# Optimization experiments

Hardware: AMD Instinct MI355X
Metric: run time of the kernel (lower is better)

Reference implementation:

```python
import jax, jax.numpy as jnp
import numpy as np

DIM = 4096
N_HEADS = 32
N_KV = 8
HEAD_DIM = 128
WINDOW = 4096
BSZ = 1
SEQ = 2048
REPEATS = N_HEADS // N_KV
SCALE = HEAD_DIM ** -0.5
NEG_INF = -1e9


def setup_inputs() -> dict:
    key = jax.random.key(0)
    ks = jax.random.split(key, 5)
    x = jax.random.normal(ks[0], (1, BSZ, SEQ, DIM), jnp.float32)
    wq = jax.random.normal(ks[1], (N_HEADS * HEAD_DIM, DIM), jnp.float32) * (DIM ** -0.5)
    wk = jax.random.normal(ks[2], (N_KV * HEAD_DIM, DIM), jnp.float32) * (DIM ** -0.5)
    wv = jax.random.normal(ks[3], (N_KV * HEAD_DIM, DIM), jnp.float32) * (DIM ** -0.5)
    wo = jax.random.normal(ks[4], (DIM, N_HEADS * HEAD_DIM), jnp.float32) * (DIM ** -0.5)
    # rotary frequencies (Mistral/LLaMA style, base 10000)
    inv = 1.0 / (10000.0 ** (np.arange(0, HEAD_DIM, 2, dtype=np.float32) / HEAD_DIM))
    ang = np.outer(np.arange(SEQ, dtype=np.float32), inv)  # [SEQ, HEAD_DIM//2]
    freqs_cos = jnp.asarray(np.cos(ang), jnp.float32)
    freqs_sin = jnp.asarray(np.sin(ang), jnp.float32)
    positions = jnp.arange(SEQ, dtype=jnp.int32)
    # sliding-window causal additive mask [SEQ, SEQ]
    i = np.arange(SEQ)[:, None]
    j = np.arange(SEQ)[None, :]
    allowed = (j <= i) & (j > i - WINDOW)
    mask = jnp.asarray(np.where(allowed, 0.0, NEG_INF).astype(np.float32))
    cache_k = jnp.zeros((BSZ, WINDOW, N_KV, HEAD_DIM), jnp.float32)
    cache_v = jnp.zeros((BSZ, WINDOW, N_KV, HEAD_DIM), jnp.float32)
    return dict(x=x, wq=wq, wk=wk, wv=wv, wo=wo, freqs_cos=freqs_cos,
                freqs_sin=freqs_sin, positions=positions, mask=mask,
                cache_k=cache_k, cache_v=cache_v)


def _rope(x, cos, sin):
    # x: [b, s, h, hd]; pairs (x0,x1),(x2,x3),... treated as complex numbers
    xr = x[..., 0::2]
    xi = x[..., 1::2]
    c = cos[None, :, None, :]
    s = sin[None, :, None, :]
    out_r = xr * c - xi * s
    out_i = xr * s + xi * c
    return jnp.stack([out_r, out_i], axis=-1).reshape(x.shape)


def reference(x, wq, wk, wv, wo, freqs_cos, freqs_sin, positions, mask, cache_k, cache_v):
    b, s = BSZ, SEQ
    xf = x.reshape(b, s, DIM)
    xq = (xf @ wq.T).reshape(b, s, N_HEADS, HEAD_DIM)
    xk = (xf @ wk.T).reshape(b, s, N_KV, HEAD_DIM)
    xv = (xf @ wv.T).reshape(b, s, N_KV, HEAD_DIM)
    xq = _rope(xq, freqs_cos, freqs_sin)
    xk = _rope(xk, freqs_cos, freqs_sin)
    # sliding-window KV cache scatter update (last WINDOW positions, mod WINDOW)
    pos = positions[-WINDOW:] % WINDOW
    cache_k = cache_k.at[:, pos].set(xk[:, -WINDOW:])
    cache_v = cache_v.at[:, pos].set(xv[:, -WINDOW:])
    # prefill branch (positions.shape[0] > 1): attend over current xk/xv
    key = jnp.repeat(xk, REPEATS, axis=2)  # GQA repeat_kv -> [b, s, H, hd]
    val = jnp.repeat(xv, REPEATS, axis=2)
    q = xq.transpose(0, 2, 1, 3)  # [b, H, s, hd]
    k = key.transpose(0, 2, 1, 3)
    v = val.transpose(0, 2, 1, 3)
    scores = jnp.einsum('bhqd,bhkd->bhqk', q, k) * SCALE + mask[None, None]
    probs = jax.nn.softmax(scores, axis=-1)
    out = jnp.einsum('bhqk,bhkd->bhqd', probs, v)
    out = out.transpose(0, 2, 1, 3).reshape(1, b, s, N_HEADS * HEAD_DIM)
    return out @ wo.T, cache_k, cache_v
```

## Files before the change

kernel.cpp:

```cpp
#include <hip/hip_runtime.h>
#include <hip/hip_bf16.h>


typedef __attribute__((ext_vector_type(8))) short short8_t;
typedef __attribute__((ext_vector_type(2))) unsigned uint2_t;
typedef __attribute__((ext_vector_type(8))) __bf16 bf16x8;
typedef __attribute__((ext_vector_type(4))) float f32x4;
typedef __attribute__((ext_vector_type(16))) float f32x16;

#define SEQLEN 2048
#define QSCALE 0.08838834764831845f

__device__ __forceinline__ short f2b(float f) {
  if (!__builtin_isfinite(f)) f = 0.0f;
  union { float f; unsigned u; } v; v.f = f;
  unsigned r = (v.u + 0x7fffu + ((v.u >> 16) & 1u)) >> 16;
  return (short)r;
}
__device__ __forceinline__ float sf(float f) {
  return __builtin_isfinite(f) ? f : 0.0f;
}
__device__ __forceinline__ short8_t cvt8(const float* p) {
  f32x4 a = *(const f32x4*)p;
  f32x4 b = *(const f32x4*)(p + 4);
  short8_t o;
  o[0] = f2b(a[0]); o[1] = f2b(a[1]); o[2] = f2b(a[2]); o[3] = f2b(a[3]);
  o[4] = f2b(b[0]); o[5] = f2b(b[1]); o[6] = f2b(b[2]); o[7] = f2b(b[3]);
  return o;
}
__device__ __forceinline__ unsigned pkb(float lo, float hi) {
  union { float f; unsigned u; } a, b; a.f = lo; b.f = hi;
  unsigned ra = (a.u + 0x7fffu + ((a.u >> 16) & 1u)) >> 16;
  unsigned rb = (b.u + 0x7fffu + ((b.u >> 16) & 1u)) & 0xffff0000u;
  return rb | ra;
}

#define GLD16(gp, lp) __builtin_amdgcn_global_load_lds( \
    (const __attribute__((address_space(1))) void*)(gp), \
    (__attribute__((address_space(3))) void*)(lp), 16, 0, 0)

__global__ __launch_bounds__(256) void cvt_bf16(
    const float* __restrict__ in, short* __restrict__ out)
{
  size_t i = ((size_t)blockIdx.x * 256 + threadIdx.x) * 8;
  *(short8_t*)&out[i] = cvt8(in + i);
}

__global__ __launch_bounds__(256) void gemm_bf(
    const short* __restrict__ A, const short* __restrict__ W,
    float* __restrict__ C0, float* __restrict__ C1,
    int Kloop, int lda, int ldc)
{
  __shared__ short As[128 * 64];
  __shared__ short Ws[128 * 64];
  const int tid  = threadIdx.x;
  const int lane = tid & 63;
  const int wid  = tid >> 6;
  const int l15  = lane & 15;
  const int l4   = lane >> 4;

  const int nwg = (int)(gridDim.x * gridDim.y);
  int bid = (int)(blockIdx.y * gridDim.x + blockIdx.x);
  int swz = (bid & 7) * (nwg >> 3) + (bid >> 3);
  const int m0 = (swz / (int)gridDim.x) * 128;
  const int n0 = (swz % (int)gridDim.x) * 128;
  const int koff = (int)blockIdx.z * Kloop;
  float* C = blockIdx.z ? C1 : C0;

  const int wr = (wid >> 1) * 64;
  const int wc = (wid & 1) * 64;
  const int srow = tid >> 3;
  const int scol = (tid & 7) * 8;

  f32x4 acc[4][4] = {};

  const short* Ab = A + (size_t)(m0 + srow) * lda + koff + scol;
  const short* Wb = W + (size_t)(n0 + srow) * lda + koff + scol;

  for (int k0 = 0; k0 < Kloop; k0 += 64) {
#pragma unroll
    for (int i = 0; i < 4; ++i) {
      GLD16(Ab + (size_t)(i * 32) * lda + k0, &As[(i * 32 + wid * 8) * 64]);
      GLD16(Wb + (size_t)(i * 32) * lda + k0, &Ws[(i * 32 + wid * 8) * 64]);
    }
    __syncthreads();

#pragma unroll
    for (int kk = 0; kk < 2; ++kk) {
      bf16x8 af[4], wf[4];
#pragma unroll
      for (int m = 0; m < 4; ++m)
        af[m] = *(const bf16x8*)&As[(wr + m * 16 + l15) * 64 + kk * 32 + l4 * 8];
#pragma unroll
      for (int n = 0; n < 4; ++n)
        wf[n] = *(const bf16x8*)&Ws[(wc + n * 16 + l15) * 64 + kk * 32 + l4 * 8];
#pragma unroll
      for (int m = 0; m < 4; ++m)
#pragma unroll
        for (int n = 0; n < 4; ++n)
          acc[m][n] = __builtin_amdgcn_mfma_f32_16x16x32_bf16(af[m], wf[n], acc[m][n], 0, 0, 0);
    }
    __syncthreads();
  }

#pragma unroll
  for (int m = 0; m < 4; ++m) {
    int rbase = m0 + wr + m * 16 + l4 * 4;
#pragma unroll
    for (int n = 0; n < 4; ++n) {
      int cbase = n0 + wc + n * 16 + l15;
#pragma unroll
      for (int r = 0; r < 4; ++r)
        C[(size_t)(rbase + r) * ldc + cbase] = sf(acc[m][n][r]);
    }
  }
}

__device__ __forceinline__ void rope8v(const float* x0, float* out,
                                       const float* fc, const float* fs, int t, int p0)
{
  f32x4 cv = *(const f32x4*)&fc[t * 64 + p0];
  f32x4 sv = *(const f32x4*)&fs[t * 64 + p0];
#pragma unroll
  for (int i = 0; i < 4; ++i) {
    float xr = x0[2 * i], xi = x0[2 * i + 1];
    out[2 * i]     = sf(xr * cv[i] - xi * sv[i]);
    out[2 * i + 1] = sf(xr * sv[i] + xi * cv[i]);
  }
}

__global__ __launch_bounds__(256) void combine_rope_q(
    const float* __restrict__ p0, const float* __restrict__ p1,
    short* __restrict__ qb, const float* __restrict__ fc, const float* __restrict__ fs)
{
  size_t idx = ((size_t)blockIdx.x * 256 + threadIdx.x) * 8;
  int t   = (int)(idx >> 12);
  int col = (int)(idx & 4095);
  f32x4 a0 = *(const f32x4*)&p0[idx],     b0 = *(const f32x4*)&p0[idx + 4];
  f32x4 a1 = *(const f32x4*)&p1[idx],     b1 = *(const f32x4*)&p1[idx + 4];
  float s8[8] = {a0[0]+a1[0], a0[1]+a1[1], a0[2]+a1[2], a0[3]+a1[3],
                 b0[0]+b1[0], b0[1]+b1[1], b0[2]+b1[2], b0[3]+b1[3]};
  float o[8];
  rope8v(s8, o, fc, fs, t, (col & 127) >> 1);
  short8_t ob;
#pragma unroll
  for (int i = 0; i < 8; ++i) ob[i] = f2b(o[i] * QSCALE);
  *(short8_t*)&qb[idx] = ob;
}

__global__ __launch_bounds__(256) void combine_rope_kv(
    const float* __restrict__ p0, const float* __restrict__ p1,
    float* __restrict__ ck, short* __restrict__ kb, float* __restrict__ cv,
    const float* __restrict__ fc, const float* __restrict__ fs)
{
  size_t idx = ((size_t)blockIdx.x * 256 + threadIdx.x) * 8;
  int t   = (int)(idx >> 11);
  int col = (int)(idx & 2047);
  f32x4 a0 = *(const f32x4*)&p0[idx],     b0 = *(const f32x4*)&p0[idx + 4];
  f32x4 a1 = *(const f32x4*)&p1[idx],     b1 = *(const f32x4*)&p1[idx + 4];
  float s8[8] = {a0[0]+a1[0], a0[1]+a1[1], a0[2]+a1[2], a0[3]+a1[3],
                 b0[0]+b1[0], b0[1]+b1[1], b0[2]+b1[2], b0[3]+b1[3]};
  if (col < 1024) {
    float o[8];
    rope8v(s8, o, fc, fs, t, (col & 127) >> 1);
    size_t di = (size_t)t * 1024 + col;
    *(f32x4*)&ck[di]     = f32x4{o[0], o[1], o[2], o[3]};
    *(f32x4*)&ck[di + 4] = f32x4{o[4], o[5], o[6], o[7]};
    short8_t ob;
#pragma unroll
    for (int i = 0; i < 8; ++i) ob[i] = f2b(o[i]);
    *(short8_t*)&kb[di] = ob;
  } else {
    size_t di = (size_t)t * 1024 + (col - 1024);
    *(f32x4*)&cv[di]     = f32x4{sf(s8[0]), sf(s8[1]), sf(s8[2]), sf(s8[3])};
    *(f32x4*)&cv[di + 4] = f32x4{sf(s8[4]), sf(s8[5]), sf(s8[6]), sf(s8[7])};
  }
}

__global__ __launch_bounds__(256) void transpose_v(
    const float* __restrict__ cv, short* __restrict__ Vt)
{
  __shared__ short tile[64][72];
  const int t0 = blockIdx.x * 64;
  const int d0 = blockIdx.y * 64;
  const int h  = blockIdx.z;
  const int tid = threadIdx.x;
  const int r = tid >> 3;
  const int c = (tid & 7) * 8;
#pragma unroll
  for (int it = 0; it < 2; ++it) {
    short8_t v = cvt8(&cv[(size_t)(t0 + it * 32 + r) * 1024 + h * 128 + d0 + c]);
    *(short8_t*)&tile[it * 32 + r][c] = v;
  }
  __syncthreads();
#pragma unroll
  for (int it = 0; it < 2; ++it) {
    int dr = it * 32 + r;
    short8_t v;
#pragma unroll
    for (int i = 0; i < 8; ++i) v[i] = tile[c + i][dr];
    *(short8_t*)&Vt[(size_t)(h * 128 + d0 + dr) * SEQLEN + t0 + c] = v;
  }
}

__global__ __launch_bounds__(256) void attn_fwd7(
    const short* __restrict__ Q,
    const short* __restrict__ Kc,
    const short* __restrict__ Vt,
    short* __restrict__ O)
{
  const int bid = (int)blockIdx.x;
  const int kvh = bid & 7;
  const int qt  = 63 - (bid >> 3);
  const int tid = (int)threadIdx.x;
  const int wid = tid >> 6;
  const int h   = kvh * 4 + wid;
  const int lane = tid & 63;
  const int l31 = lane & 31;
  const int hi  = lane >> 5;

  __shared__ short Ks[64 * 128];
  __shared__ short Vs[128 * 64];
  __shared__ short P[4][32][72];
  __shared__ float exch[4][32];

  const int q0 = qt * 32;
  const int qg = q0 + l31;
  const int kend = q0 + 32;

  bf16x8 qf[8];
  {
    const short* qp = Q + (size_t)qg * 4096 + h * 128 + hi * 8;
#pragma unroll
    for (int ks = 0; ks < 8; ++ks) qf[ks] = *(const bf16x8*)(qp + ks * 16);
  }

  f32x16 o0 = {}, o1 = {}, o2 = {}, o3 = {};
  float m = -1e30f, l = 0.f;

  const int krow_base = wid * 16;
  const int vrow_base = wid * 32;
  const int xk = l31 & 15;
  const int xv = l31 & 7;

  for (int kt = 0; kt < kend; kt += 64) {
#pragma unroll
    for (int it = 0; it < 4; ++it) {
      int krow = krow_base + it * 4 + (lane >> 4);
      int kch  = (lane & 15) ^ (krow & 15);
      GLD16(Kc + (size_t)(kt + krow) * 1024 + kvh * 128 + kch * 8,
            &Ks[wid * 2048 + it * 512]);
      int vrow = vrow_base + it * 8 + (lane >> 3);
      int vch  = (lane & 7) ^ (vrow & 7);
      GLD16(Vt + (size_t)(kvh * 128 + vrow) * SEQLEN + kt + vch * 8,
            &Vs[wid * 2048 + it * 512]);
    }
    __syncthreads();

    f32x16 s0 = {}, s1 = {};
    {
      __builtin_amdgcn_s_setprio(1);
#pragma unroll
      for (int ks = 0; ks < 8; ++ks) {
        int ch = (ks * 2 + hi) ^ xk;
        bf16x8 k0 = *(const bf16x8*)&Ks[l31 * 128 + ch * 8];
        bf16x8 k1 = *(const bf16x8*)&Ks[(32 + l31) * 128 + ch * 8];
        s0 = __builtin_amdgcn_mfma_f32_32x32x16_bf16(k0, qf[ks], s0, 0, 0, 0);
        s1 = __builtin_amdgcn_mfma_f32_32x32x16_bf16(k1, qf[ks], s1, 0, 0, 0);
      }
      __builtin_amdgcn_s_setprio(0);
    }

    if (kt + 63 > q0) {
#pragma unroll
      for (int r = 0; r < 16; ++r) {
        int crow = (r & 3) + 8 * (r >> 2) + 4 * hi;
        if (kt + crow > qg)      s0[r] = -1e30f;
        if (kt + 32 + crow > qg) s1[r] = -1e30f;
      }
    }
    {
      float t[8];
#pragma unroll
      for (int r = 0; r < 8; ++r)
        t[r] = fmaxf(fmaxf(s0[r], s0[r + 8]), fmaxf(s1[r], s1[r + 8]));
      float pmax = fmaxf(fmaxf(fmaxf(t[0], t[1]), fmaxf(t[2], t[3])),
                         fmaxf(fmaxf(t[4], t[5]), fmaxf(t[6], t[7])));
      pmax = fmaxf(pmax, __shfl_xor(pmax, 32, 64));
      if (!__all(pmax <= m + 8.f)) {
        float mnew = fmaxf(m, pmax);
        float resc = __expf(m - mnew);
        m = mnew; l *= resc;
        if (lane < 32) exch[wid][l31] = resc;
#pragma unroll
        for (int r = 0; r < 16; ++r) {
          float rs = exch[wid][(r & 3) + 8 * (r >> 2) + 4 * hi];
          o0[r] *= rs; o1[r] *= rs; o2[r] *= rs; o3[r] *= rs;
        }
      }
      float psum = 0.f;
#pragma unroll
      for (int r = 0; r < 16; ++r) { s0[r] = __expf(s0[r] - m); psum += s0[r]; }
#pragma unroll
      for (int r = 0; r < 16; ++r) { s1[r] = __expf(s1[r] - m); psum += s1[r]; }
      l += psum + __shfl_xor(psum, 32, 64);
#pragma unroll
      for (int t4 = 0; t4 < 4; ++t4) {
        int c = 8 * t4 + 4 * hi;
        *(uint2_t*)&P[wid][l31][c]      = uint2_t{pkb(s0[4*t4], s0[4*t4+1]), pkb(s0[4*t4+2], s0[4*t4+3])};
        *(uint2_t*)&P[wid][l31][32 + c] = uint2_t{pkb(s1[4*t4], s1[4*t4+1]), pkb(s1[4*t4+2], s1[4*t4+3])};
      }
    }

#pragma unroll
    for (int g = 0; g < 4; ++g) {
      int ch = (g * 2 + hi) ^ xv;
      bf16x8 vf0 = *(const bf16x8*)&Vs[(l31)      * 64 + ch * 8];
      bf16x8 vf1 = *(const bf16x8*)&Vs[(32 + l31) * 64 + ch * 8];
      bf16x8 vf2 = *(const bf16x8*)&Vs[(64 + l31) * 64 + ch * 8];
      bf16x8 vf3 = *(const bf16x8*)&Vs[(96 + l31) * 64 + ch * 8];
      bf16x8 pf  = *(const bf16x8*)&P[wid][l31][g * 16 + hi * 8];
      __builtin_amdgcn_s_setprio(1);
      o0 = __builtin_amdgcn_mfma_f32_32x32x16_bf16(pf, vf0, o0, 0, 0, 0);
      o1 = __builtin_amdgcn_mfma_f32_32x32x16_bf16(pf, vf1, o1, 0, 0, 0);
      o2 = __builtin_amdgcn_mfma_f32_32x32x16_bf16(pf, vf2, o2, 0, 0, 0);
      o3 = __builtin_amdgcn_mfma_f32_32x32x16_bf16(pf, vf3, o3, 0, 0, 0);
      __builtin_amdgcn_s_setprio(0);
    }
    __syncthreads();
  }

  if (lane < 32) exch[wid][l31] = 1.f / l;
#pragma unroll
  for (int r = 0; r < 16; ++r) {
    int crow = (r & 3) + 8 * (r >> 2) + 4 * hi;
    float inv = exch[wid][crow];
    short* ob = O + (size_t)(q0 + crow) * 4096 + h * 128 + l31;
    ob[0]  = f2b(o0[r] * inv);
    ob[32] = f2b(o1[r] * inv);
    ob[64] = f2b(o2[r] * inv);
    ob[96] = f2b(o3[r] * inv);
  }
}

extern "C" void kernel_launch(void* const* d_in, const int* in_sizes, int n_in,
                              void* d_out, int out_size, void* d_ws, size_t ws_size,
                              hipStream_t stream) {
  const float* x  = (const float*)d_in[0];
  const float* wq = (const float*)d_in[1];
  const float* wk = (const float*)d_in[2];
  const float* wv = (const float*)d_in[3];
  const float* wo = (const float*)d_in[4];
  const float* fc = (const float*)d_in[5];
  const float* fs = (const float*)d_in[6];

  float* out = (float*)d_out;
  float* out_main = out;
  float* cache_k  = out + (size_t)2048 * 4096;
  float* cache_v  = cache_k + (size_t)4096 * 8 * 128;

  short* slotA = (short*)d_ws;
  short* slotB = (short*)((char*)d_ws + 33554432);
  short* Vt    = (short*)((char*)d_ws + 33554432 + 16777216);
  short* x_bf  = slotB;
  short* attn_out = slotB;
  short* q_bf  = slotA;
  short* wkv_bf = slotA + (size_t)2048 * 4096;
  short* k_bf  = slotA + (size_t)2048 * 4096;

  float* pQ0 = out_main;
  float* pQ1 = cache_k;
  float* pKV0 = out_main;
  float* pKV1 = out_main + (size_t)2048 * 2048;

  cvt_bf16<<<4096, 256, 0, stream>>>(x, x_bf);
  cvt_bf16<<<8192, 256, 0, stream>>>(wq, slotA);
  gemm_bf<<<dim3(32, 16, 2), 256, 0, stream>>>(x_bf, slotA, pQ0, pQ1, 2048, 4096, 4096);
  combine_rope_q<<<4096, 256, 0, stream>>>(pQ0, pQ1, q_bf, fc, fs);

  cvt_bf16<<<2048, 256, 0, stream>>>(wk, wkv_bf);
  cvt_bf16<<<2048, 256, 0, stream>>>(wv, wkv_bf + (size_t)1024 * 4096);
  gemm_bf<<<dim3(16, 16, 2), 256, 0, stream>>>(x_bf, wkv_bf, pKV0, pKV1, 2048, 4096, 2048);
  combine_rope_kv<<<2048, 256, 0, stream>>>(pKV0, pKV1, cache_k, k_bf, cache_v, fc, fs);
  transpose_v<<<dim3(32, 2, 8), 256, 0, stream>>>(cache_v, Vt);
  hipMemsetAsync(cache_k + (size_t)2048 * 1024, 0, (size_t)2048 * 1024 * 4, stream);
  hipMemsetAsync(cache_v + (size_t)2048 * 1024, 0, (size_t)2048 * 1024 * 4, stream);

  attn_fwd7<<<512, 256, 0, stream>>>(q_bf, k_bf, Vt, attn_out);

  cvt_bf16<<<8192, 256, 0, stream>>>(wo, slotA);
  gemm_bf<<<dim3(32, 16, 1), 256, 0, stream>>>(attn_out, slotA, out_main, out_main, 4096, 4096, 4096);
}
```

Before: 424.0 us.

## Fuse RoPE epilogue into projection GEMMs, drop split-K, double-buffer LDS

Drops the split-K (z=2) partial-sum scheme for the Q and KV projections. RoPE, the Q scale, and the bf16/fp32 cache writes now happen in the GEMM epilogue, using a lane shuffle to pair real and imaginary parts. This removes the two combine kernels and their fp32 partial round-trips. It also double-buffers the LDS tiles so the next K-slice loads are issued before computing on the current one. The cost is fewer workgroups for the QKV GEMMs (512 and 256 instead of 1024 and 512), which can lower occupancy and CU utilisation, plus doubled shared memory.

```diff
diff --git a/kernel.cpp b/kernel.cpp
--- a/kernel.cpp
+++ b/kernel.cpp
@@ -46,13 +46,15 @@
   *(short8_t*)&out[i] = cvt8(in + i);
 }
 
-__global__ __launch_bounds__(256) void gemm_bf(
+template <int EPI>
+__global__ __launch_bounds__(256) void gemm_epi(
     const short* __restrict__ A, const short* __restrict__ W,
-    float* __restrict__ C0, float* __restrict__ C1,
-    int Kloop, int lda, int ldc)
+    float* __restrict__ C, short* __restrict__ Cb, float* __restrict__ C2,
+    const float* __restrict__ fc, const float* __restrict__ fs,
+    int K, int ldc)
 {
-  __shared__ short As[128 * 64];
-  __shared__ short Ws[128 * 64];
+  __shared__ short As[2][128 * 64];
+  __shared__ short Ws[2][128 * 64];
   const int tid  = threadIdx.x;
   const int lane = tid & 63;
   const int wid  = tid >> 6;
@@ -64,8 +66,6 @@
   int swz = (bid & 7) * (nwg >> 3) + (bid >> 3);
   const int m0 = (swz / (int)gridDim.x) * 128;
   const int n0 = (swz % (int)gridDim.x) * 128;
-  const int koff = (int)blockIdx.z * Kloop;
-  float* C = blockIdx.z ? C1 : C0;
 
   const int wr = (wid >> 1) * 64;
   const int wc = (wid & 1) * 64;
@@ -74,26 +74,34 @@
 
   f32x4 acc[4][4] = {};
 
-  const short* Ab = A + (size_t)(m0 + srow) * lda + koff + scol;
-  const short* Wb = W + (size_t)(n0 + srow) * lda + koff + scol;
-
-  for (int k0 = 0; k0 < Kloop; k0 += 64) {
-#pragma unroll
-    for (int i = 0; i < 4; ++i) {
-      GLD16(Ab + (size_t)(i * 32) * lda + k0, &As[(i * 32 + wid * 8) * 64]);
-      GLD16(Wb + (size_t)(i * 32) * lda + k0, &Ws[(i * 32 + wid * 8) * 64]);
-    }
-    __syncthreads();
-
+  const short* Ab = A + (size_t)(m0 + srow) * K + scol;
+  const short* Wb = W + (size_t)(n0 + srow) * K + scol;
+
+#pragma unroll
+  for (int i = 0; i < 4; ++i) {
+    GLD16(Ab + (size_t)(i * 32) * K, &As[0][(i * 32 + wid * 8) * 64]);
+    GLD16(Wb + (size_t)(i * 32) * K, &Ws[0][(i * 32 + wid * 8) * 64]);
+  }
+  __syncthreads();
+
+  int cur = 0;
+  for (int k0 = 0; k0 < K; k0 += 64) {
+    if (k0 + 64 < K) {
+#pragma unroll
+      for (int i = 0; i < 4; ++i) {
+        GLD16(Ab + (size_t)(i * 32) * K + k0 + 64, &As[cur ^ 1][(i * 32 + wid * 8) * 64]);
+        GLD16(Wb + (size_t)(i * 32) * K + k0 + 64, &Ws[cur ^ 1][(i * 32 + wid * 8) * 64]);
+      }
+    }
 #pragma unroll
     for (int kk = 0; kk < 2; ++kk) {
       bf16x8 af[4], wf[4];
 #pragma unroll
       for (int m = 0; m < 4; ++m)
-        af[m] = *(const bf16x8*)&As[(wr + m * 16 + l15) * 64 + kk * 32 + l4 * 8];
+        af[m] = *(const bf16x8*)&As[cur][(wr + m * 16 + l15) * 64 + kk * 32 + l4 * 8];
 #pragma unroll
       for (int n = 0; n < 4; ++n)
-        wf[n] = *(const bf16x8*)&Ws[(wc + n * 16 + l15) * 64 + kk * 32 + l4 * 8];
+        wf[n] = *(const bf16x8*)&Ws[cur][(wc + n * 16 + l15) * 64 + kk * 32 + l4 * 8];
 #pragma unroll
       for (int m = 0; m < 4; ++m)
 #pragma unroll
@@ -101,6 +109,7 @@
           acc[m][n] = __builtin_amdgcn_mfma_f32_16x16x32_bf16(af[m], wf[n], acc[m][n], 0, 0, 0);
     }
     __syncthreads();
+    cur ^= 1;
   }
 
 #pragma unroll
@@ -110,70 +119,29 @@
     for (int n = 0; n < 4; ++n) {
       int cbase = n0 + wc + n * 16 + l15;
 #pragma unroll
-      for (int r = 0; r < 4; ++r)
-        C[(size_t)(rbase + r) * ldc + cbase] = sf(acc[m][n][r]);
-    }
-  }
-}
-
-__device__ __forceinline__ void rope8v(const float* x0, float* out,
-                                       const float* fc, const float* fs, int t, int p0)
-{
-  f32x4 cv = *(const f32x4*)&fc[t * 64 + p0];
-  f32x4 sv = *(const f32x4*)&fs[t * 64 + p0];
-#pragma unroll
-  for (int i = 0; i < 4; ++i) {
-    float xr = x0[2 * i], xi = x0[2 * i + 1];
-    out[2 * i]     = sf(xr * cv[i] - xi * sv[i]);
-    out[2 * i + 1] = sf(xr * sv[i] + xi * cv[i]);
-  }
-}
-
-__global__ __launch_bounds__(256) void combine_rope_q(
-    const float* __restrict__ p0, const float* __restrict__ p1,
-    short* __restrict__ qb, const float* __restrict__ fc, const float* __restrict__ fs)
-{
-  size_t idx = ((size_t)blockIdx.x * 256 + threadIdx.x) * 8;
-  int t   = (int)(idx >> 12);
-  int col = (int)(idx & 4095);
-  f32x4 a0 = *(const f32x4*)&p0[idx],     b0 = *(const f32x4*)&p0[idx + 4];
-  f32x4 a1 = *(const f32x4*)&p1[idx],     b1 = *(const f32x4*)&p1[idx + 4];
-  float s8[8] = {a0[0]+a1[0], a0[1]+a1[1], a0[2]+a1[2], a0[3]+a1[3],
-                 b0[0]+b1[0], b0[1]+b1[1], b0[2]+b1[2], b0[3]+b1[3]};
-  float o[8];
-  rope8v(s8, o, fc, fs, t, (col & 127) >> 1);
-  short8_t ob;
-#pragma unroll
-  for (int i = 0; i < 8; ++i) ob[i] = f2b(o[i] * QSCALE);
-  *(short8_t*)&qb[idx] = ob;
-}
-
-__global__ __launch_bounds__(256) void combine_rope_kv(
-    const float* __restrict__ p0, const float* __restrict__ p1,
-    float* __restrict__ ck, short* __restrict__ kb, float* __restrict__ cv,
-    const float* __restrict__ fc, const float* __restrict__ fs)
-{
-  size_t idx = ((size_t)blockIdx.x * 256 + threadIdx.x) * 8;
-  int t   = (int)(idx >> 11);
-  int col = (int)(idx & 2047);
-  f32x4 a0 = *(const f32x4*)&p0[idx],     b0 = *(const f32x4*)&p0[idx + 4];
-  f32x4 a1 = *(const f32x4*)&p1[idx],     b1 = *(const f32x4*)&p1[idx + 4];
-  float s8[8] = {a0[0]+a1[0], a0[1]+a1[1], a0[2]+a1[2], a0[3]+a1[3],
-                 b0[0]+b1[0], b0[1]+b1[1], b0[2]+b1[2], b0[3]+b1[3]};
-  if (col < 1024) {
-    float o[8];
-    rope8v(s8, o, fc, fs, t, (col & 127) >> 1);
-    size_t di = (size_t)t * 1024 + col;
-    *(f32x4*)&ck[di]     = f32x4{o[0], o[1], o[2], o[3]};
-    *(f32x4*)&ck[di + 4] = f32x4{o[4], o[5], o[6], o[7]};
-    short8_t ob;
-#pragma unroll
-    for (int i = 0; i < 8; ++i) ob[i] = f2b(o[i]);
-    *(short8_t*)&kb[di] = ob;
-  } else {
-    size_t di = (size_t)t * 1024 + (col - 1024);
-    *(f32x4*)&cv[di]     = f32x4{sf(s8[0]), sf(s8[1]), sf(s8[2]), sf(s8[3])};
-    *(f32x4*)&cv[di + 4] = f32x4{sf(s8[4]), sf(s8[5]), sf(s8[6]), sf(s8[7])};
+      for (int r = 0; r < 4; ++r) {
+        float x = acc[m][n][r];
+        if (EPI == 0) {
+          C[(size_t)(rbase + r) * ldc + cbase] = sf(x);
+        } else {
+          float xp = __shfl_xor(x, 1, 64);
+          int row = rbase + r;
+          int p = (cbase & 127) >> 1;
+          float c = fc[row * 64 + p], s = fs[row * 64 + p];
+          float o = (l15 & 1) ? (xp * s + x * c) : (x * c - xp * s);
+          if (EPI == 1) {
+            Cb[(size_t)row * 4096 + cbase] = f2b(o * QSCALE);
+          } else {
+            if (cbase < 1024) {
+              C[(size_t)row * 1024 + cbase]  = sf(o);
+              Cb[(size_t)row * 1024 + cbase] = f2b(o);
+            } else {
+              C2[(size_t)row * 1024 + cbase - 1024] = sf(x);
+            }
+          }
+        }
+      }
+    }
   }
 }
 
@@ -364,24 +332,17 @@
   short* Vt    = (short*)((char*)d_ws + 33554432 + 16777216);
   short* x_bf  = slotB;
   short* attn_out = slotB;
-  short* q_bf  = slotA;
-  short* wkv_bf = slotA + (size_t)2048 * 4096;
-  short* k_bf  = slotA + (size_t)2048 * 4096;
-
-  float* pQ0 = out_main;
-  float* pQ1 = cache_k;
-  float* pKV0 = out_main;
-  float* pKV1 = out_main + (size_t)2048 * 2048;
+
+  short* q_bf = (short*)out_main;
+  short* k_bf = q_bf + (size_t)2048 * 4096;
 
   cvt_bf16<<<4096, 256, 0, stream>>>(x, x_bf);
   cvt_bf16<<<8192, 256, 0, stream>>>(wq, slotA);
-  gemm_bf<<<dim3(32, 16, 2), 256, 0, stream>>>(x_bf, slotA, pQ0, pQ1, 2048, 4096, 4096);
-  combine_rope_q<<<4096, 256, 0, stream>>>(pQ0, pQ1, q_bf, fc, fs);
-
-  cvt_bf16<<<2048, 256, 0, stream>>>(wk, wkv_bf);
-  cvt_bf16<<<2048, 256, 0, stream>>>(wv, wkv_bf + (size_t)1024 * 4096);
-  gemm_bf<<<dim3(16, 16, 2), 256, 0, stream>>>(x_bf, wkv_bf, pKV0, pKV1, 2048, 4096, 2048);
-  combine_rope_kv<<<2048, 256, 0, stream>>>(pKV0, pKV1, cache_k, k_bf, cache_v, fc, fs);
+  gemm_epi<1><<<dim3(32, 16), 256, 0, stream>>>(x_bf, slotA, nullptr, q_bf, nullptr, fc, fs, 4096, 0);
+
+  cvt_bf16<<<2048, 256, 0, stream>>>(wk, slotA);
+  cvt_bf16<<<2048, 256, 0, stream>>>(wv, slotA + (size_t)1024 * 4096);
+  gemm_epi<2><<<dim3(16, 16), 256, 0, stream>>>(x_bf, slotA, cache_k, k_bf, cache_v, fc, fs, 4096, 0);
   transpose_v<<<dim3(32, 2, 8), 256, 0, stream>>>(cache_v, Vt);
   hipMemsetAsync(cache_k + (size_t)2048 * 1024, 0, (size_t)2048 * 1024 * 4, stream);
   hipMemsetAsync(cache_v + (size_t)2048 * 1024, 0, (size_t)2048 * 1024 * 4, stream);
@@ -389,5 +350,5 @@
   attn_fwd7<<<512, 256, 0, stream>>>(q_bf, k_bf, Vt, attn_out);
 
   cvt_bf16<<<8192, 256, 0, stream>>>(wo, slotA);
-  gemm_bf<<<dim3(32, 16, 1), 256, 0, stream>>>(attn_out, slotA, out_main, out_main, 4096, 4096, 4096);
-}
+  gemm_epi<0><<<dim3(32, 16), 256, 0, stream>>>(attn_out, slotA, out_main, nullptr, nullptr, nullptr, nullptr, 4096, 4096);
+}
```

New measurement: 450.2 us. 1.06x slower.
